# Performance work log

Measured on AMD Instinct MI355X. Metric: run time of the kernel, lower is better.

## Reference

```python
import jax, jax.numpy as jnp
import numpy as np

N_EMBD = 1024
N_HEAD = 16
HEAD_DIM = N_EMBD // N_HEAD
EPS = 1e-5


def _gelu_tanh(x):
    c = jnp.sqrt(jnp.asarray(2.0 / jnp.pi, x.dtype))
    return 0.5 * x * (1.0 + jnp.tanh(c * (x + 0.044715 * x ** 3)))


def _layernorm(x, scale, shift):
    # torch.var defaults to unbiased (ddof=1) -- replicate exactly
    mean = jnp.mean(x, axis=-1, keepdims=True)
    var = jnp.var(x, axis=-1, keepdims=True, ddof=1)
    return (x - mean) / jnp.sqrt(var + EPS) * scale + shift


def setup_inputs() -> dict:
    key = jax.random.key(0)
    ks = jax.random.split(key, 8)
    d, h = N_EMBD, 4 * N_EMBD
    s = 0.02
    return {
        "x": jax.random.normal(ks[0], (2, 2048, d), jnp.float32),
        "ln1_scale": jnp.ones((d,), jnp.float32),
        "ln1_shift": jnp.zeros((d,), jnp.float32),
        "wq": jax.random.normal(ks[1], (d, d), jnp.float32) * s,
        "wk": jax.random.normal(ks[2], (d, d), jnp.float32) * s,
        "wv": jax.random.normal(ks[3], (d, d), jnp.float32) * s,
        "w_out": jax.random.normal(ks[4], (d, d), jnp.float32) * s,
        "b_out": jnp.zeros((d,), jnp.float32),
        "ln2_scale": jnp.ones((d,), jnp.float32),
        "ln2_shift": jnp.zeros((d,), jnp.float32),
        "w1": jax.random.normal(ks[5], (d, h), jnp.float32) * s,
        "b1": jnp.zeros((h,), jnp.float32),
        "w2": jax.random.normal(ks[6], (h, d), jnp.float32) * s,
        "b2": jnp.zeros((d,), jnp.float32),
    }


def reference(x, ln1_scale, ln1_shift, wq, wk, wv, w_out, b_out,
              ln2_scale, ln2_shift, w1, b1, w2, b2):
    B, S, D = x.shape
    out = _layernorm(x, ln1_scale, ln1_shift)

    # qkv projections (no bias), split heads: [B, H, S, hd]
    q = (out @ wq).reshape(B, S, N_HEAD, HEAD_DIM).transpose(0, 2, 1, 3)
    k = (out @ wk).reshape(B, S, N_HEAD, HEAD_DIM).transpose(0, 2, 1, 3)
    v = (out @ wv).reshape(B, S, N_HEAD, HEAD_DIM).transpose(0, 2, 1, 3)

    scores = jnp.einsum("bhqd,bhkd->bhqk", q, k)
    causal = jnp.triu(jnp.ones((S, S), bool), k=1)
    # original masks BEFORE scaling; -inf / sqrt(d) is still -inf
    scores = jnp.where(causal, -jnp.inf, scores)
    weights = jax.nn.softmax(scores / jnp.sqrt(jnp.asarray(HEAD_DIM, scores.dtype)), axis=-1)
    ctx = jnp.einsum("bhqk,bhkd->bqhd", weights, v).reshape(B, S, D)
    attn_out = ctx @ w_out + b_out

    out = attn_out + x  # dropout is identity (rate 0)
    shortcut = out
    out = _layernorm(out, ln2_scale, ln2_shift)
    out = _gelu_tanh(out @ w1 + b1) @ w2 + b2
    return out + shortcut
```

## Files before the change

### kernel.cpp

```cpp
#include <hip/hip_runtime.h>
#include <stdint.h>
#include <math.h>

using bf16x8 = __attribute__((ext_vector_type(8))) short;
using f32x4  = __attribute__((ext_vector_type(4))) float;

__device__ __forceinline__ uint16_t f2b(float f) {
    union { float f; uint32_t i; } v; v.f = f;
    uint32_t r = v.i + 0x7fffu + ((v.i >> 16) & 1u);
    return (uint16_t)(r >> 16);
}
__device__ __forceinline__ float b2f(uint16_t u) {
    union { uint32_t i; float f; } v; v.i = ((uint32_t)u) << 16; return v.f;
}

typedef const __attribute__((address_space(1))) void gvoid;
typedef __attribute__((address_space(3))) void svoid;

__global__ __launch_bounds__(256) void fill_zero(float* __restrict__ o, int n) {
    int i = (blockIdx.x * 256 + threadIdx.x) * 4;
    if (i < n) *(float4*)(o + i) = make_float4(0.f, 0.f, 0.f, 0.f);
}

__global__ __launch_bounds__(256) void transpose_qkvo(
    const float* __restrict__ wq, const float* __restrict__ wk,
    const float* __restrict__ wv, const float* __restrict__ wo,
    uint16_t* __restrict__ wqkvT, uint16_t* __restrict__ woT)
{
    const int D = 1024;
    int z = blockIdx.z;
    const float* W = (z == 0) ? wq : (z == 1) ? wk : (z == 2) ? wv : wo;
    uint16_t* Wt = (z < 3) ? (wqkvT + (size_t)z * D * D) : woT;
    __shared__ uint16_t t[32][33];
    int n0 = blockIdx.x * 32, k0 = blockIdx.y * 32;
    int tx = threadIdx.x, ty = threadIdx.y;
    #pragma unroll
    for (int i = ty; i < 32; i += 8)
        t[i][tx] = f2b(W[(size_t)(k0 + i) * D + (n0 + tx)]);
    __syncthreads();
    #pragma unroll
    for (int i = ty; i < 32; i += 8)
        Wt[(size_t)(n0 + i) * D + (k0 + tx)] = t[tx][i];
}

__global__ __launch_bounds__(256) void transpose_f2b(
    const float* __restrict__ W, uint16_t* __restrict__ Wt, int K, int N)
{
    __shared__ uint16_t t[32][33];
    int n0 = blockIdx.x * 32, k0 = blockIdx.y * 32;
    int tx = threadIdx.x, ty = threadIdx.y;
    #pragma unroll
    for (int i = ty; i < 32; i += 8)
        t[i][tx] = f2b(W[(size_t)(k0 + i) * N + (n0 + tx)]);
    __syncthreads();
    #pragma unroll
    for (int i = ty; i < 32; i += 8)
        Wt[(size_t)(n0 + i) * K + (k0 + tx)] = t[tx][i];
}

__global__ __launch_bounds__(256) void ln_kernel(
    const float* __restrict__ src, const float* __restrict__ scale,
    const float* __restrict__ shift, uint16_t* __restrict__ out)
{
    const int D = 1024;
    int row = blockIdx.x, t = threadIdx.x;
    float4 f = *((const float4*)(src + (size_t)row * D) + t);
    float v[4] = {f.x, f.y, f.z, f.w};
    float s1 = v[0] + v[1] + v[2] + v[3];
    float s2 = v[0]*v[0] + v[1]*v[1] + v[2]*v[2] + v[3]*v[3];
    #pragma unroll
    for (int off = 32; off; off >>= 1) {
        s1 += __shfl_xor(s1, off);
        s2 += __shfl_xor(s2, off);
    }
    __shared__ float red[2][4];
    __shared__ float stat[2];
    int wid = t >> 6, lane = t & 63;
    if (lane == 0) { red[0][wid] = s1; red[1][wid] = s2; }
    __syncthreads();
    if (t == 0) {
        float S1 = red[0][0] + red[0][1] + red[0][2] + red[0][3];
        float S2 = red[1][0] + red[1][1] + red[1][2] + red[1][3];
        float mean = S1 / (float)D;
        float var  = fmaxf((S2 - mean * S1) / (float)(D - 1), 0.f);
        stat[0] = mean; stat[1] = rsqrtf(var + 1e-5f);
    }
    __syncthreads();
    float mean = stat[0], rstd = stat[1];
    float4 sc = *((const float4*)scale + t);
    float4 sh = *((const float4*)shift + t);
    uint16_t o[4];
    o[0] = f2b((v[0] - mean) * rstd * sc.x + sh.x);
    o[1] = f2b((v[1] - mean) * rstd * sc.y + sh.y);
    o[2] = f2b((v[2] - mean) * rstd * sc.z + sh.z);
    o[3] = f2b((v[3] - mean) * rstd * sc.w + sh.w);
    uint2 st;
    st.x = (uint32_t)o[0] | ((uint32_t)o[1] << 16);
    st.y = (uint32_t)o[2] | ((uint32_t)o[3] << 16);
    *(uint2*)(out + (size_t)row * D + t * 4) = st;
}

__global__ __launch_bounds__(256) void combine2(
    float* __restrict__ dst, const float* __restrict__ part0,
    const float* __restrict__ resid, const float* __restrict__ bias)
{
    const int D = 1024;
    size_t o = (size_t)blockIdx.x * D + threadIdx.x * 4;
    float4 a = *(float4*)(dst + o);
    float4 b = *(const float4*)(part0 + o);
    float4 c = *(const float4*)(resid + o);
    float4 bv = *((const float4*)bias + threadIdx.x);
    a.x += b.x + c.x + bv.x;
    a.y += b.y + c.y + bv.y;
    a.z += b.z + c.z + bv.z;
    a.w += b.w + c.w + bv.w;
    *(float4*)(dst + o) = a;
}

__global__ __launch_bounds__(256) void combine2ln(
    float* __restrict__ res1, const float* __restrict__ part0,
    const float* __restrict__ x, const float* __restrict__ bo,
    const float* __restrict__ scale, const float* __restrict__ shift,
    uint16_t* __restrict__ out)
{
    const int D = 1024;
    int row = blockIdx.x, t = threadIdx.x;
    size_t o = (size_t)row * D + t * 4;
    float4 a = *(float4*)(res1 + o);
    float4 b = *(const float4*)(part0 + o);
    float4 c = *(const float4*)(x + o);
    float4 bv = *((const float4*)bo + t);
    float v[4] = {a.x + b.x + c.x + bv.x, a.y + b.y + c.y + bv.y,
                  a.z + b.z + c.z + bv.z, a.w + b.w + c.w + bv.w};
    *(float4*)(res1 + o) = make_float4(v[0], v[1], v[2], v[3]);

    float s1 = v[0] + v[1] + v[2] + v[3];
    float s2 = v[0]*v[0] + v[1]*v[1] + v[2]*v[2] + v[3]*v[3];
    #pragma unroll
    for (int off = 32; off; off >>= 1) {
        s1 += __shfl_xor(s1, off);
        s2 += __shfl_xor(s2, off);
    }
    __shared__ float red[2][4];
    __shared__ float stat[2];
    int wid = t >> 6, lane = t & 63;
    if (lane == 0) { red[0][wid] = s1; red[1][wid] = s2; }
    __syncthreads();
    if (t == 0) {
        float S1 = red[0][0] + red[0][1] + red[0][2] + red[0][3];
        float S2 = red[1][0] + red[1][1] + red[1][2] + red[1][3];
        float mean = S1 / (float)D;
        float var  = fmaxf((S2 - mean * S1) / (float)(D - 1), 0.f);
        stat[0] = mean; stat[1] = rsqrtf(var + 1e-5f);
    }
    __syncthreads();
    float mean = stat[0], rstd = stat[1];
    float4 sc = *((const float4*)scale + t);
    float4 sh = *((const float4*)shift + t);
    uint16_t ob[4];
    ob[0] = f2b((v[0] - mean) * rstd * sc.x + sh.x);
    ob[1] = f2b((v[1] - mean) * rstd * sc.y + sh.y);
    ob[2] = f2b((v[2] - mean) * rstd * sc.z + sh.z);
    ob[3] = f2b((v[3] - mean) * rstd * sc.w + sh.w);
    uint2 st;
    st.x = (uint32_t)ob[0] | ((uint32_t)ob[1] << 16);
    st.y = (uint32_t)ob[2] | ((uint32_t)ob[3] << 16);
    *(uint2*)(out + (size_t)row * D + t * 4) = st;
}

__device__ __forceinline__ void stage128(
    const uint16_t* __restrict__ A, const uint16_t* __restrict__ Bt,
    uint16_t* As, uint16_t* Bs,
    int m0, int n0, int lda, int kk, int w, int l)
{
    int srow = l >> 3;
    int sc = ((l & 7) ^ srow) << 3;
    #pragma unroll
    for (int p = 0; p < 4; ++p) {
        int rbase = w * 32 + p * 8;
        const uint16_t* ga = A  + (size_t)(m0 + rbase + srow) * lda + kk + sc;
        const uint16_t* gb = Bt + (size_t)(n0 + rbase + srow) * lda + kk + sc;
        __builtin_amdgcn_global_load_lds((gvoid*)ga, (svoid*)(As + rbase * 64), 16, 0, 0);
        __builtin_amdgcn_global_load_lds((gvoid*)gb, (svoid*)(Bs + rbase * 64), 16, 0, 0);
    }
}

__device__ __forceinline__ void comp128(
    const uint16_t* As, const uint16_t* Bs, f32x4 (&acc)[4][4],
    int mo, int no, int quad, int ln, int sw)
{
    #pragma unroll
    for (int s = 0; s < 2; ++s) {
        int cc = ((s * 64 + quad * 16) ^ sw) >> 1;
        bf16x8 af[4], bf[4];
        #pragma unroll
        for (int i = 0; i < 4; ++i)
            af[i] = *(const bf16x8*)(As + (mo + i * 16 + ln) * 64 + cc);
        #pragma unroll
        for (int i = 0; i < 4; ++i)
            bf[i] = *(const bf16x8*)(Bs + (no + i * 16 + ln) * 64 + cc);
        #pragma unroll
        for (int mi = 0; mi < 4; ++mi)
            #pragma unroll
            for (int ni = 0; ni < 4; ++ni)
                acc[mi][ni] = __builtin_amdgcn_mfma_f32_16x16x32_bf16(
                    af[mi], bf[ni], acc[mi][ni], 0, 0, 0);
    }
}

template <int EPI>
__global__ __launch_bounds__(256) void gemm128(
    const uint16_t* __restrict__ A, const uint16_t* __restrict__ Bt,
    const float* __restrict__ bias, const float* __restrict__ resid,
    void* __restrict__ outp, void* __restrict__ out2,
    int M, int N, int K, int lda)
{
    __shared__ __align__(16) uint16_t As0[128 * 64];
    __shared__ __align__(16) uint16_t As1[128 * 64];
    __shared__ __align__(16) uint16_t Bs0[128 * 64];
    __shared__ __align__(16) uint16_t Bs1[128 * 64];
    int tid = threadIdx.x;
    int w = tid >> 6, l = tid & 63;
    int quad = l >> 4, ln = l & 15;
    int sw = (ln & 7) << 4;

    int Nt = gridDim.x, Mt = gridDim.y;
    int L0 = blockIdx.y * Nt + blockIdx.x;
    int nb = Nt * Mt;
    int L = (L0 & 7) * (nb >> 3) + (L0 >> 3);
    const int GROUP = 8;
    int nig = GROUP * Nt;
    int gid = L / nig;
    int fm = gid * GROUP;
    int gsz = min(Mt - fm, GROUP);
    int rem = L - gid * nig;
    int pid_m = fm + rem % gsz;
    int pid_n = rem / gsz;
    int n0 = pid_n * 128, m0 = pid_m * 128;
    int kofs = (EPI == 5) ? blockIdx.z * K : 0;

    int mo = (w & 1) * 64, no = (w >> 1) * 64;

    f32x4 acc[4][4];
    #pragma unroll
    for (int mi = 0; mi < 4; ++mi)
        #pragma unroll
        for (int ni = 0; ni < 4; ++ni) acc[mi][ni] = (f32x4){0.f, 0.f, 0.f, 0.f};

    int nk = K >> 6;
    stage128(A, Bt, As0, Bs0, m0, n0, lda, kofs, w, l);
    __syncthreads();

    for (int t = 0; t + 2 <= nk; t += 2) {
        stage128(A, Bt, As1, Bs1, m0, n0, lda, kofs + (t + 1) * 64, w, l);
        comp128(As0, Bs0, acc, mo, no, quad, ln, sw);
        __syncthreads();
        if (t + 2 < nk)
            stage128(A, Bt, As0, Bs0, m0, n0, lda, kofs + (t + 2) * 64, w, l);
        comp128(As1, Bs1, acc, mo, no, quad, ln, sw);
        if (t + 2 < nk) __syncthreads();
    }

    float* pout = (EPI == 5) ? (blockIdx.z ? (float*)out2 : (float*)outp) : (float*)outp;

    #pragma unroll
    for (int ni = 0; ni < 4; ++ni) {
        int col = n0 + no + ni * 16 + ln;
        if (EPI == 4 && col >= 2048) {
            int hh = (col - 2048) >> 6, d = (col - 2048) & 63;
            #pragma unroll
            for (int mi = 0; mi < 4; ++mi) {
                int tok = m0 + mo + mi * 16 + quad * 4;
                int bat = tok >> 11, s = tok & 2047;
                uint16_t pk[4];
                #pragma unroll
                for (int r = 0; r < 4; ++r) pk[r] = f2b(acc[mi][ni][r]);
                uint2 st;
                st.x = (uint32_t)pk[0] | ((uint32_t)pk[1] << 16);
                st.y = (uint32_t)pk[2] | ((uint32_t)pk[3] << 16);
                *(uint2*)((uint16_t*)out2 +
                          ((size_t)(bat * 16 + hh) * 64 + d) * 2048 + s) = st;
            }
            continue;
        }
        float bv = (EPI == 1 || EPI == 2) ? bias[col] : 0.f;
        #pragma unroll
        for (int mi = 0; mi < 4; ++mi) {
            #pragma unroll
            for (int r = 0; r < 4; ++r) {
                int row = m0 + mo + mi * 16 + quad * 4 + r;
                float vacc = acc[mi][ni][r] + bv;
                if (EPI == 1) {
                    size_t idx = (size_t)row * N + col;
                    ((float*)outp)[idx] = vacc + resid[idx];
                } else if (EPI == 5) {
                    pout[(size_t)row * N + col] = vacc;
                } else if (EPI == 2) {
                    float x = vacc;
                    float u = 0.7978845608028654f * (x + 0.044715f * x * x * x);
                    float g = x / (1.f + __expf(-2.f * u));
                    ((uint16_t*)outp)[(size_t)row * N + col] = f2b(g);
                } else {
                    float vs = (col < 1024) ? vacc * 0.125f : vacc;
                    ((uint16_t*)outp)[(size_t)(col >> 10) * M * 1024 +
                                      (size_t)row * 1024 + (col & 1023)] = f2b(vs);
                }
            }
        }
    }
}

__device__ __forceinline__ void attn_tile(
    const uint16_t* __restrict__ Kl, const uint16_t* __restrict__ Vl,
    uint16_t* __restrict__ Pw,
    bf16x8 qf0, bf16x8 qf1,
    float* l_r, f32x4* o_acc,
    int qw, int kv0, bool diag, int quad, int ln)
{
    const int LW = 72;
    f32x4 sf[4];
    #pragma unroll
    for (int nt2 = 0; nt2 < 4; ++nt2) {
        const uint16_t* kp = Kl + (nt2 * 16 + ln) * LW + quad * 8;
        bf16x8 k0 = *(const bf16x8*)(kp);
        bf16x8 k1 = *(const bf16x8*)(kp + 32);
        f32x4 z = {0.f, 0.f, 0.f, 0.f};
        z = __builtin_amdgcn_mfma_f32_16x16x32_bf16(qf0, k0, z, 0, 0, 0);
        z = __builtin_amdgcn_mfma_f32_16x16x32_bf16(qf1, k1, z, 0, 0, 0);
        sf[nt2] = z;
    }
    #pragma unroll
    for (int r = 0; r < 4; ++r) {
        float ps = 0.f;
        if (diag) {
            int qrow = qw + quad * 4 + r;
            #pragma unroll
            for (int nt2 = 0; nt2 < 4; ++nt2) {
                int kv = kv0 + nt2 * 16 + ln;
                float pv = (kv <= qrow) ? __expf(sf[nt2][r]) : 0.f;
                sf[nt2][r] = pv;
                ps += pv;
            }
        } else {
            #pragma unroll
            for (int nt2 = 0; nt2 < 4; ++nt2) {
                float pv = __expf(sf[nt2][r]);
                sf[nt2][r] = pv;
                ps += pv;
            }
        }
        ps += __shfl_xor(ps, 1);
        ps += __shfl_xor(ps, 2);
        ps += __shfl_xor(ps, 4);
        ps += __shfl_xor(ps, 8);
        l_r[r] += ps;
    }
    #pragma unroll
    for (int nt2 = 0; nt2 < 4; ++nt2) {
        int gl = nt2 * 2 + (ln >> 3);
        int off = ln & 7;
        #pragma unroll
        for (int r = 0; r < 4; ++r) {
            int row = quad * 4 + r;
            int p = gl ^ ((quad << 1) ^ r);
            Pw[row * 64 + p * 8 + off] = f2b(sf[nt2][r]);
        }
    }
    int swl = ((ln >> 2) << 1) ^ (ln & 3);
    int g0 = quad ^ swl;
    int g1 = (quad + 4) ^ swl;
    bf16x8 p0 = *(const bf16x8*)(Pw + ln * 64 + g0 * 8);
    bf16x8 p1 = *(const bf16x8*)(Pw + ln * 64 + g1 * 8);
    #pragma unroll
    for (int dt = 0; dt < 4; ++dt) {
        const uint16_t* vp = Vl + (dt * 16 + ln) * LW + quad * 8;
        bf16x8 v0 = *(const bf16x8*)(vp);
        bf16x8 v1 = *(const bf16x8*)(vp + 32);
        o_acc[dt] = __builtin_amdgcn_mfma_f32_16x16x32_bf16(p0, v0, o_acc[dt], 0, 0, 0);
        o_acc[dt] = __builtin_amdgcn_mfma_f32_16x16x32_bf16(p1, v1, o_acc[dt], 0, 0, 0);
    }
}

__global__ __launch_bounds__(256) void attn_flash(
    const uint16_t* __restrict__ Q,
    const uint16_t* __restrict__ K,
    const uint16_t* __restrict__ Vt,
    uint16_t* __restrict__ O,
    int B, int S, int H)
{
    const int D = 1024;
    const int LW = 72;
    __shared__ uint16_t Kl[64 * 72];
    __shared__ uint16_t Vl[64 * 72];
    __shared__ uint16_t Pl[64 * 64];

    int tid = threadIdx.x;
    int w = tid >> 6, l = tid & 63;
    int quad = l >> 4, ln = l & 15;

    int NT = S / 64;
    int qlo = blockIdx.x;
    int qhi = NT - 1 - qlo;
    int h = blockIdx.y, b = blockIdx.z;
    size_t rb = (size_t)b * S;

    int qwl = qlo * 64 + w * 16;
    int qwh = qhi * 64 + w * 16;

    const uint16_t* qpl = Q + (rb + qwl + ln) * D + h * 64 + quad * 8;
    bf16x8 ql0 = *(const bf16x8*)(qpl);
    bf16x8 ql1 = *(const bf16x8*)(qpl + 32);
    const uint16_t* qph = Q + (rb + qwh + ln) * D + h * 64 + quad * 8;
    bf16x8 qh0 = *(const bf16x8*)(qph);
    bf16x8 qh1 = *(const bf16x8*)(qph + 32);

    const uint16_t* Kbase = K + rb * D + h * 64;
    const uint16_t* Vbase = Vt + (size_t)(b * H + h) * 64 * S;
    uint16_t* Pw = Pl + w * 16 * 64;

    int sr0 = tid >> 3,         sc0 = (tid & 7) * 8;
    int sr1 = (256 + tid) >> 3, sc1 = ((256 + tid) & 7) * 8;

    float lL[4] = {0.f, 0.f, 0.f, 0.f};
    float lH[4] = {0.f, 0.f, 0.f, 0.f};
    f32x4 oL[4], oH[4];
    #pragma unroll
    for (int dt = 0; dt < 4; ++dt) {
        oL[dt] = (f32x4){0.f, 0.f, 0.f, 0.f};
        oH[dt] = (f32x4){0.f, 0.f, 0.f, 0.f};
    }

    uint4 kr0 = *(const uint4*)(Kbase + (size_t)sr0 * D + sc0);
    uint4 kr1 = *(const uint4*)(Kbase + (size_t)sr1 * D + sc1);
    uint4 vr0 = *(const uint4*)(Vbase + (size_t)sr0 * S + sc0);
    uint4 vr1 = *(const uint4*)(Vbase + (size_t)sr1 * S + sc1);

    for (int t = 0; t <= qhi; ++t) {
        __syncthreads();
        *(uint4*)(Kl + sr0 * LW + sc0) = kr0;
        *(uint4*)(Kl + sr1 * LW + sc1) = kr1;
        *(uint4*)(Vl + sr0 * LW + sc0) = vr0;
        *(uint4*)(Vl + sr1 * LW + sc1) = vr1;
        __syncthreads();
        if (t < qhi) {
            int kv1 = (t + 1) * 64;
            kr0 = *(const uint4*)(Kbase + (size_t)(kv1 + sr0) * D + sc0);
            kr1 = *(const uint4*)(Kbase + (size_t)(kv1 + sr1) * D + sc1);
            vr0 = *(const uint4*)(Vbase + (size_t)sr0 * S + kv1 + sc0);
            vr1 = *(const uint4*)(Vbase + (size_t)sr1 * S + kv1 + sc1);
        }
        int kv0 = t * 64;
        attn_tile(Kl, Vl, Pw, qh0, qh1, lH, oH, qwh, kv0, t == qhi, quad, ln);
        if (t <= qlo)
            attn_tile(Kl, Vl, Pw, ql0, ql1, lL, oL, qwl, kv0, t == qlo, quad, ln);
    }

    #pragma unroll
    for (int r = 0; r < 4; ++r) {
        float invH = 1.f / lH[r];
        float invL = 1.f / lL[r];
        uint16_t* oph = O + (rb + qwh + quad * 4 + r) * D + h * 64 + ln;
        uint16_t* opl = O + (rb + qwl + quad * 4 + r) * D + h * 64 + ln;
        #pragma unroll
        for (int dt = 0; dt < 4; ++dt) {
            oph[dt * 16] = f2b(oH[dt][r] * invH);
            opl[dt * 16] = f2b(oL[dt][r] * invL);
        }
    }
}

extern "C" void kernel_launch(void* const* d_in, const int* in_sizes, int n_in,
                              void* d_out, int out_size, void* d_ws, size_t ws_size,
                              hipStream_t stream)
{
    (void)in_sizes; (void)n_in;
    const int B = 2, S = 2048, D = 1024, H = 16, F = 4096;
    const int M = B * S;
    const size_t MB = 1u << 20;

    const float* x    = (const float*)d_in[0];
    const float* ln1s = (const float*)d_in[1];
    const float* ln1b = (const float*)d_in[2];
    const float* wq   = (const float*)d_in[3];
    const float* wk   = (const float*)d_in[4];
    const float* wv   = (const float*)d_in[5];
    const float* wo   = (const float*)d_in[6];
    const float* bo   = (const float*)d_in[7];
    const float* ln2s = (const float*)d_in[8];
    const float* ln2b = (const float*)d_in[9];
    const float* w1   = (const float*)d_in[10];
    const float* b1   = (const float*)d_in[11];
    const float* w2   = (const float*)d_in[12];
    const float* b2   = (const float*)d_in[13];

    if (ws_size < 56 * MB) {
        fill_zero<<<(out_size + 1023) / 1024, 256, 0, stream>>>((float*)d_out, out_size);
        return;
    }
    bool full = ws_size >= 72 * MB;

    char* base = (char*)d_ws;
    uint16_t* woT    = (uint16_t*)(base + 0 * MB);
    uint16_t* wqkvT  = (uint16_t*)(base + 2 * MB);
    uint16_t* ln1o   = (uint16_t*)(base + 8 * MB);
    uint16_t* qb     = (uint16_t*)(base + 16 * MB);
    uint16_t* vbT    = (uint16_t*)(base + 32 * MB);
    uint16_t* ctx    = (uint16_t*)(base + 40 * MB);
    uint16_t* kb     = (uint16_t*)(base + 24 * MB);
    uint16_t* w1T    = (uint16_t*)(base + 0 * MB);
    float*    res1   = (float*)   (base + (full ? 56 : 16) * MB);
    uint16_t* ln2o   = (uint16_t*)(base + (full ? 8 : 32) * MB);
    uint16_t* w2T    = (uint16_t*)(base + (full ? 16 : 40) * MB);
    uint16_t* h1     = (uint16_t*)(base + (full ? 24 : 48) * MB);
    float*    part0  = (float*)   (base + 0 * MB);
    float*    partP  = (float*)   (base + 8 * MB);

    dim3 tb(32, 8);
    transpose_qkvo<<<dim3(D / 32, D / 32, 4), tb, 0, stream>>>(
        wq, wk, wv, wo, wqkvT, woT);

    ln_kernel<<<M, 256, 0, stream>>>(x, ln1s, ln1b, ln1o);

    gemm128<4><<<dim3(3072 / 128, M / 128), 256, 0, stream>>>(
        ln1o, wqkvT, nullptr, nullptr, qb, vbT, M, 3072, D, D);

    attn_flash<<<dim3(S / 128, H, B), 256, 0, stream>>>(qb, kb, vbT, ctx, B, S, H);

    if (full) {
        gemm128<5><<<dim3(D / 128, M / 128, 2), 256, 0, stream>>>(
            ctx, woT, nullptr, nullptr, partP, res1, M, D, D / 2, D);
        combine2ln<<<M, 256, 0, stream>>>(res1, partP, x, bo, ln2s, ln2b, ln2o);
    } else {
        gemm128<1><<<dim3(D / 128, M / 128), 256, 0, stream>>>(
            ctx, woT, bo, x, res1, nullptr, M, D, D, D);
        ln_kernel<<<M, 256, 0, stream>>>(res1, ln2s, ln2b, ln2o);
    }

    transpose_f2b<<<dim3(F / 32, D / 32), tb, 0, stream>>>(w1, w1T, D, F);
    transpose_f2b<<<dim3(D / 32, F / 32), tb, 0, stream>>>(w2, w2T, F, D);

    if (full) {
        gemm128<2><<<dim3(F / 128, M / 128), 256, 0, stream>>>(
            ln2o, w1T, b1, nullptr, h1, nullptr, M, F, D, D);
        gemm128<5><<<dim3(D / 128, M / 128, 2), 256, 0, stream>>>(
            h1, w2T, nullptr, nullptr, part0, d_out, M, D, F / 2, F);
        combine2<<<M, 256, 0, stream>>>((float*)d_out, part0, res1, b2);
    } else {
        const int MH = M / 2;
        for (int half = 0; half < 2; ++half) {
            size_t ro = (size_t)half * MH;
            gemm128<2><<<dim3(F / 128, MH / 128), 256, 0, stream>>>(
                ln2o + ro * D, w1T, b1, nullptr, h1, nullptr, MH, F, D, D);
            gemm128<1><<<dim3(D / 128, MH / 128), 256, 0, stream>>>(
                h1, w2T, b2, res1 + ro * D, (float*)d_out + ro * D, nullptr, MH, D, F, F);
        }
    }
}
```

Before: 349.2 us.

## Process one query tile per attention block instead of paired lo/hi tiles

```diff
diff --git a/kernel.cpp b/kernel.cpp
--- a/kernel.cpp
+++ b/kernel.cpp
@@ -399,20 +399,15 @@
     int quad = l >> 4, ln = l & 15;
 
     int NT = S / 64;
-    int qlo = blockIdx.x;
-    int qhi = NT - 1 - qlo;
     int h = blockIdx.y, b = blockIdx.z;
+    int qt = ((h >> 3) & 1) ? blockIdx.x : (NT - 1 - blockIdx.x);
     size_t rb = (size_t)b * S;
 
-    int qwl = qlo * 64 + w * 16;
-    int qwh = qhi * 64 + w * 16;
-
-    const uint16_t* qpl = Q + (rb + qwl + ln) * D + h * 64 + quad * 8;
-    bf16x8 ql0 = *(const bf16x8*)(qpl);
-    bf16x8 ql1 = *(const bf16x8*)(qpl + 32);
-    const uint16_t* qph = Q + (rb + qwh + ln) * D + h * 64 + quad * 8;
-    bf16x8 qh0 = *(const bf16x8*)(qph);
-    bf16x8 qh1 = *(const bf16x8*)(qph + 32);
+    int qw = qt * 64 + w * 16;
+
+    const uint16_t* qp = Q + (rb + qw + ln) * D + h * 64 + quad * 8;
+    bf16x8 q0 = *(const bf16x8*)(qp);
+    bf16x8 q1 = *(const bf16x8*)(qp + 32);
 
     const uint16_t* Kbase = K + rb * D + h * 64;
     const uint16_t* Vbase = Vt + (size_t)(b * H + h) * 64 * S;
@@ -421,51 +416,41 @@
     int sr0 = tid >> 3,         sc0 = (tid & 7) * 8;
     int sr1 = (256 + tid) >> 3, sc1 = ((256 + tid) & 7) * 8;
 
-    float lL[4] = {0.f, 0.f, 0.f, 0.f};
-    float lH[4] = {0.f, 0.f, 0.f, 0.f};
-    f32x4 oL[4], oH[4];
-    #pragma unroll
-    for (int dt = 0; dt < 4; ++dt) {
-        oL[dt] = (f32x4){0.f, 0.f, 0.f, 0.f};
-        oH[dt] = (f32x4){0.f, 0.f, 0.f, 0.f};
-    }
+    float lr[4] = {0.f, 0.f, 0.f, 0.f};
+    f32x4 oa[4];
+    #pragma unroll
+    for (int dt = 0; dt < 4; ++dt)
+        oa[dt] = (f32x4){0.f, 0.f, 0.f, 0.f};
 
     uint4 kr0 = *(const uint4*)(Kbase + (size_t)sr0 * D + sc0);
     uint4 kr1 = *(const uint4*)(Kbase + (size_t)sr1 * D + sc1);
     uint4 vr0 = *(const uint4*)(Vbase + (size_t)sr0 * S + sc0);
     uint4 vr1 = *(const uint4*)(Vbase + (size_t)sr1 * S + sc1);
 
-    for (int t = 0; t <= qhi; ++t) {
+    for (int t = 0; t <= qt; ++t) {
         __syncthreads();
         *(uint4*)(Kl + sr0 * LW + sc0) = kr0;
         *(uint4*)(Kl + sr1 * LW + sc1) = kr1;
         *(uint4*)(Vl + sr0 * LW + sc0) = vr0;
         *(uint4*)(Vl + sr1 * LW + sc1) = vr1;
         __syncthreads();
-        if (t < qhi) {
+        if (t < qt) {
             int kv1 = (t + 1) * 64;
             kr0 = *(const uint4*)(Kbase + (size_t)(kv1 + sr0) * D + sc0);
             kr1 = *(const uint4*)(Kbase + (size_t)(kv1 + sr1) * D + sc1);
             vr0 = *(const uint4*)(Vbase + (size_t)sr0 * S + kv1 + sc0);
             vr1 = *(const uint4*)(Vbase + (size_t)sr1 * S + kv1 + sc1);
         }
-        int kv0 = t * 64;
-        attn_tile(Kl, Vl, Pw, qh0, qh1, lH, oH, qwh, kv0, t == qhi, quad, ln);
-        if (t <= qlo)
-            attn_tile(Kl, Vl, Pw, ql0, ql1, lL, oL, qwl, kv0, t == qlo, quad, ln);
+        attn_tile(Kl, Vl, Pw, q0, q1, lr, oa, qw, t * 64, t == qt, quad, ln);
     }
 
     #pragma unroll
     for (int r = 0; r < 4; ++r) {
-        float invH = 1.f / lH[r];
-        float invL = 1.f / lL[r];
-        uint16_t* oph = O + (rb + qwh + quad * 4 + r) * D + h * 64 + ln;
-        uint16_t* opl = O + (rb + qwl + quad * 4 + r) * D + h * 64 + ln;
-        #pragma unroll
-        for (int dt = 0; dt < 4; ++dt) {
-            oph[dt * 16] = f2b(oH[dt][r] * invH);
-            opl[dt * 16] = f2b(oL[dt][r] * invL);
-        }
+        float inv = 1.f / lr[r];
+        uint16_t* op = O + (rb + qw + quad * 4 + r) * D + h * 64 + ln;
+        #pragma unroll
+        for (int dt = 0; dt < 4; ++dt)
+            op[dt * 16] = f2b(oa[dt][r] * inv);
     }
 }
 
@@ -524,7 +509,7 @@
     gemm128<4><<<dim3(3072 / 128, M / 128), 256, 0, stream>>>(
         ln1o, wqkvT, nullptr, nullptr, qb, vbT, M, 3072, D, D);
 
-    attn_flash<<<dim3(S / 128, H, B), 256, 0, stream>>>(qb, kb, vbT, ctx, B, S, H);
+    attn_flash<<<dim3(S / 64, H, B), 256, 0, stream>>>(qb, kb, vbT, ctx, B, S, H);
 
     if (full) {
         gemm128<5><<<dim3(D / 128, M / 128, 2), 256, 0, stream>>>(
```

Result: slower. 363.6 us (+4.1%).
